# Performance work log

Hardware: AMD Instinct MI355X
Metric: run time of the kernel (lower is better)

## Reference

```python
import jax, jax.numpy as jnp
import numpy as np


def setup_inputs() -> dict:
    key = jax.random.key(0)
    kx, kd = jax.random.split(key)
    B, T, C = 32, 512, 512
    x = jax.random.normal(kx, (B, T, C), dtype=jnp.float32)
    dur = jax.random.randint(kd, (B, T), 0, 12, dtype=jnp.int32)
    return {"x": x, "dur": dur}


def reference(x, dur):
    # x: [B, T, C]; dur: [B, T] integer per-token durations.
    # Equivalent of the torch CPU double-loop: output frame t of row b
    # takes source index j where cumsum(dur)[b, j-1] <= t < cumsum(dur)[b, j];
    # frames past the total duration repeat the last source index (T-1).
    dur = jnp.maximum(dur, 0)
    cum = jnp.cumsum(dur, axis=1)                       # [B, T], nondecreasing
    T_out = int(jnp.max(cum))                            # data-dependent output length (eager)
    frames = jnp.arange(T_out, dtype=cum.dtype)          # [T_out]
    # searchsorted(cum[b], t, 'right') == first j with cum[b, j] > t
    idx = jax.vmap(lambda c: jnp.searchsorted(c, frames, side="right"))(cum)  # [B, T_out]
    idx = jnp.minimum(idx, x.shape[1] - 1)               # overflow -> last token, matches torch loop
    return jnp.take_along_axis(x, idx[:, :, None], axis=1)  # [B, T_out, C]
```

## Files before the change

### kernel.cpp

```cpp
#include <hip/hip_runtime.h>
#include <hip/hip_bf16.h>


#define LR_T   512
#define NTAIL  64

typedef float vfloat4 __attribute__((ext_vector_type(4)));

__global__ void lr_cumsum_kernel(const int* __restrict__ dur,
                                 int* __restrict__ cum, int T) {
    __shared__ int s[LR_T];
    const int b = blockIdx.x;
    const int tid = threadIdx.x;
    int v = dur[(size_t)b * T + tid];
    v = v > 0 ? v : 0;
    s[tid] = v;
    __syncthreads();
    for (int off = 1; off < LR_T; off <<= 1) {
        int add = (tid >= off) ? s[tid - off] : 0;
        __syncthreads();
        s[tid] += add;
        __syncthreads();
    }
    cum[(size_t)b * T + tid] = s[tid];
}

__global__ void __launch_bounds__(256)
lr_scatter_kernel(const vfloat4* __restrict__ x4,
                  const int* __restrict__ cum,
                  vfloat4* __restrict__ out4,
                  int T, int T_out) {
    const int jj   = blockIdx.x;
    const int b    = blockIdx.y;
    const int tid  = threadIdx.x;
    const int lane = tid & 127;
    const int half = tid >> 7;

    const int* crow = cum + (size_t)b * T;
    int j, start, end;
    if (jj < T) {
        j = jj;
        if (jj > 0) {
            const int2 se = *(const int2*)(crow + jj - 1);
            start = se.x;
            end   = se.y;
        } else {
            start = 0;
            end   = crow[0];
        }
    } else {
        j = T - 1;
        const int tstart = crow[T - 1];
        const int tlen   = T_out - tstart;
        if (tlen <= 0) return;
        const int chunk = (tlen + NTAIL - 1) / NTAIL;
        const int k     = jj - T;
        start = tstart + k * chunk;
        end   = start + chunk;
        if (end > T_out) end = T_out;
    }
    if (start >= end) return;

    const vfloat4 val =
        __builtin_nontemporal_load(&x4[((size_t)b * T + j) * 128 + lane]);

    vfloat4* const base = out4 + (size_t)b * T_out * 128 + lane;
    vfloat4* dst = base + ((size_t)start + half) * 128;
    for (int t = start + half; t < end; t += 2) {
        __builtin_nontemporal_store(val, dst);
        dst += 256;
    }
}

extern "C" void kernel_launch(void* const* d_in, const int* in_sizes, int n_in,
                              void* d_out, int out_size, void* d_ws, size_t ws_size,
                              hipStream_t stream) {
    const float* x   = (const float*)d_in[0];
    const int*   dur = (const int*)d_in[1];
    float*       out = (float*)d_out;

    const int B  = 32;
    const int BT = in_sizes[1];
    const int T  = BT / B;
    const int C  = in_sizes[0] / BT;
    const int T_out = out_size / (B * C);

    int* cum = (int*)d_ws;

    lr_cumsum_kernel<<<B, T, 0, stream>>>(dur, cum, T);

    dim3 grid(T + NTAIL, B);
    lr_scatter_kernel<<<grid, 256, 0, stream>>>(
        (const vfloat4*)x, cum, (vfloat4*)out, T, T_out);
}
```

Before: 231.2 us.

## Replace per-token scatter with per-frame gather using shared-memory binary search

Switches from one block per source token that scatters its row over its duration range to blocks that each own 64 output frames. Each block loads the row's cumsum into shared memory, binary-searches the source index for each frame, then gathers rows from x with regular loads and nontemporal stores. This aims to balance work evenly across blocks, where the old scheme had very uneven per-token durations and idle empty-duration blocks. In exchange, x rows are reread once per frame instead of once per token, which relies on cache hits, and every block repeats the 2KB cumsum load and a search.

```diff
diff --git a/kernel.cpp b/kernel.cpp
--- a/kernel.cpp
+++ b/kernel.cpp
@@ -1,9 +1,8 @@
 #include <hip/hip_runtime.h>
-#include <hip/hip_bf16.h>
 
 
-#define LR_T   512
-#define NTAIL  64
+#define LR_T 512
+#define FPB  64
 
 typedef float vfloat4 __attribute__((ext_vector_type(4)));
 
@@ -26,49 +25,41 @@
 }
 
 __global__ void __launch_bounds__(256)
-lr_scatter_kernel(const vfloat4* __restrict__ x4,
-                  const int* __restrict__ cum,
-                  vfloat4* __restrict__ out4,
-                  int T, int T_out) {
-    const int jj   = blockIdx.x;
-    const int b    = blockIdx.y;
-    const int tid  = threadIdx.x;
+lr_gather_kernel(const vfloat4* __restrict__ x4,
+                 const int* __restrict__ cum,
+                 vfloat4* __restrict__ out4,
+                 int T_out) {
+    __shared__ int s_cum[LR_T];
+    __shared__ int s_idx[FPB];
+    const int tid = threadIdx.x;
+    const int b   = blockIdx.y;
+    const int t0  = blockIdx.x * FPB;
+
+    const int* crow = cum + (size_t)b * LR_T;
+    s_cum[tid]       = crow[tid];
+    s_cum[tid + 256] = crow[tid + 256];
+    __syncthreads();
+
+    const int nf = min(FPB, T_out - t0);
+
+    if (tid < nf) {
+        const int t = t0 + tid;
+        int pos = 0;
+        #pragma unroll
+        for (int s = LR_T / 2; s > 0; s >>= 1)
+            pos += (s_cum[pos + s - 1] <= t) ? s : 0;
+        s_idx[tid] = pos;
+    }
+    __syncthreads();
+
     const int lane = tid & 127;
     const int half = tid >> 7;
-
-    const int* crow = cum + (size_t)b * T;
-    int j, start, end;
-    if (jj < T) {
-        j = jj;
-        if (jj > 0) {
-            const int2 se = *(const int2*)(crow + jj - 1);
-            start = se.x;
-            end   = se.y;
-        } else {
-            start = 0;
-            end   = crow[0];
-        }
-    } else {
-        j = T - 1;
-        const int tstart = crow[T - 1];
-        const int tlen   = T_out - tstart;
-        if (tlen <= 0) return;
-        const int chunk = (tlen + NTAIL - 1) / NTAIL;
-        const int k     = jj - T;
-        start = tstart + k * chunk;
-        end   = start + chunk;
-        if (end > T_out) end = T_out;
-    }
-    if (start >= end) return;
-
-    const vfloat4 val =
-        __builtin_nontemporal_load(&x4[((size_t)b * T + j) * 128 + lane]);
-
-    vfloat4* const base = out4 + (size_t)b * T_out * 128 + lane;
-    vfloat4* dst = base + ((size_t)start + half) * 128;
-    for (int t = start + half; t < end; t += 2) {
-        __builtin_nontemporal_store(val, dst);
-        dst += 256;
+    const vfloat4* __restrict__ xrow = x4 + (size_t)b * LR_T * 128 + lane;
+    vfloat4* __restrict__ obase = out4 + ((size_t)b * T_out + t0) * 128 + lane;
+    #pragma unroll 4
+    for (int f = half; f < nf; f += 2) {
+        const vfloat4 v = xrow[(size_t)s_idx[f] * 128];
+        __builtin_nontemporal_store(v, obase + (size_t)f * 128);
     }
 }
 
@@ -89,7 +80,9 @@
 
     lr_cumsum_kernel<<<B, T, 0, stream>>>(dur, cum, T);
 
-    dim3 grid(T + NTAIL, B);
-    lr_scatter_kernel<<<grid, 256, 0, stream>>>(
-        (const vfloat4*)x, cum, (vfloat4*)out, T, T_out);
+    if (T_out > 0) {
+        dim3 grid((T_out + FPB - 1) / FPB, B);
+        lr_gather_kernel<<<grid, 256, 0, stream>>>(
+            (const vfloat4*)x, cum, (vfloat4*)out, T_out);
+    }
 }
```

Result: slower. 239.3 us (+3.5%).
